# Performance work log

Measured on AMD Instinct MI355X. Metric: run time of the kernel, lower is better.

The kernel has to match this reference:

```python
import jax, jax.numpy as jnp
import numpy as np
from jax import lax

EPS = 1e-5  # BatchNorm eps (eval mode, running stats)
HEADS = 8

# --- surrogate-gradient Heaviside (sigmoid surrogate, alpha=4) ---
@jax.custom_vjp
def spike(u):
    return (u >= 0.0).astype(u.dtype)

def _spike_fwd(u):
    return spike(u), u

def _spike_bwd(u, g):
    s = jax.nn.sigmoid(4.0 * u)
    return (g * 4.0 * s * (1.0 - s),)

spike.defvjp(_spike_fwd, _spike_bwd)

def lif(x, tau=0.5, threshold=1.0):
    """Multi-step LIF over leading time axis: v_t = tau*v_{t-1} + x_t,
    s_t = H(v_t - threshold), hard reset v_t *= (1 - s_t)."""
    def step(v, xt):
        v = tau * v + xt
        s = spike(v - threshold)
        return v * (1.0 - s), s
    _, out = lax.scan(step, jnp.zeros_like(x[0]), x)
    return out

def bn_eval(x, gamma, beta, mean, var):
    # x: (T,B,C,N); per-channel affine using running stats
    inv = gamma / jnp.sqrt(var + EPS)
    return x * inv[None, None, :, None] + (beta - mean * inv)[None, None, :, None]

def setup_inputs() -> dict:
    key = jax.random.key(0)
    ks = jax.random.split(key, 12)
    T, B, C, H, W = 4, 32, 384, 16, 16
    d = {}
    d['x'] = jax.random.normal(ks[0], (T, B, C, H, W), dtype=jnp.float32)
    # 1x1 Conv1d weights == (C_out, C_in) matrices
    sc = 1.0 / np.sqrt(C)
    d['q_w'] = jax.random.normal(ks[1], (C, C), dtype=jnp.float32) * sc
    d['q_gamma'] = jnp.ones((C,), jnp.float32)
    d['q_beta'] = jnp.zeros((C,), jnp.float32)
    d['q_mean'] = jax.random.normal(ks[2], (C,), dtype=jnp.float32) * 0.1
    d['q_var'] = jax.random.uniform(ks[3], (C,), dtype=jnp.float32) + 0.5
    d['k_w'] = jax.random.normal(ks[4], (C, C), dtype=jnp.float32) * sc
    d['k_gamma'] = jnp.ones((C,), jnp.float32)
    d['k_beta'] = jnp.zeros((C,), jnp.float32)
    d['k_mean'] = jax.random.normal(ks[5], (C,), dtype=jnp.float32) * 0.1
    d['k_var'] = jax.random.uniform(ks[6], (C,), dtype=jnp.float32) + 0.5
    d['proj_w'] = jax.random.normal(ks[7], (C, C), dtype=jnp.float32) * sc
    d['proj_b'] = jax.random.normal(ks[8], (C,), dtype=jnp.float32) * 0.01
    d['proj_gamma'] = jnp.ones((C,), jnp.float32)
    d['proj_beta'] = jnp.zeros((C,), jnp.float32)
    d['proj_mean'] = jax.random.normal(ks[9], (C,), dtype=jnp.float32) * 0.1
    d['proj_var'] = jax.random.uniform(ks[10], (C,), dtype=jnp.float32) + 0.5
    d['mem_alpha'] = jnp.float32(0.2)
    return d

def reference(x, q_w, q_gamma, q_beta, q_mean, q_var,
              k_w, k_gamma, k_beta, k_mean, k_var,
              proj_w, proj_b, proj_gamma, proj_beta, proj_mean, proj_var,
              mem_alpha):
    T, B, C, H, W = x.shape
    Hh = HEADS
    Dh = C // Hh
    N = H * W
    # proj_lif applied to raw input, then flatten spatial dims
    s = lif(x, tau=0.5, threshold=1.0).reshape(T, B, C, N)
    # q path: 1x1 conv (channel GEMM) -> BN -> LIF
    q = lif(bn_eval(jnp.einsum('tbcn,dc->tbdn', s, q_w), q_gamma, q_beta, q_mean, q_var),
            tau=0.5, threshold=1.0).reshape(T, B, Hh, Dh, N)
    # k path
    k = lif(bn_eval(jnp.einsum('tbcn,dc->tbdn', s, k_w), k_gamma, k_beta, k_mean, k_var),
            tau=0.5, threshold=1.0).reshape(T, B, Hh, Dh, N)
    # temporal decayed memory: m_0 = q_0; m_t = alpha*m_{t-1} + (1-alpha)*q_{t-1}
    def mstep(m_prev, q_prev):
        m = mem_alpha * m_prev + (1.0 - mem_alpha) * q_prev
        return m, m
    _, mems_rest = lax.scan(mstep, q[0], q[:-1])
    mems = jnp.concatenate([q[:1], mems_rest], axis=0)  # (T,B,Hh,Dh,N)
    # cat along Dh then sum == sum(mems)+sum(q)
    q_sum = jnp.sum(mems, axis=3, keepdims=True) + jnp.sum(q, axis=3, keepdims=True)
    attn = lif(q_sum, tau=0.5, threshold=0.5)  # (T,B,Hh,1,N)
    y = (attn * k).reshape(T, B, C, N)
    # proj conv (with bias) -> BN -> reshape back to (T,B,C,H,W)
    y = jnp.einsum('tbcn,dc->tbdn', y, proj_w) + proj_b[None, None, :, None]
    y = bn_eval(y, proj_gamma, proj_beta, proj_mean, proj_var)
    return y.reshape(T, B, C, H, W)
```

## Files before the change

kernel.cpp:

```cpp
#include <hip/hip_runtime.h>

#define T_ 4
#define B_ 32
#define C_ 384
#define N_ 256
#define HEADS_ 8
#define DH_ 48
#define EPS_ 1e-5f
#define NW_ (C_*C_)

typedef _Float16 f16;
typedef __attribute__((ext_vector_type(8))) _Float16 f16x8;
typedef __attribute__((ext_vector_type(16))) float f32x16;

#define PSCALE     4096.0f
#define PSCALE_INV (1.0f/4096.0f)
#define SPIKE_BYTE 0x3Cu

__device__ __forceinline__ void unpack4(unsigned int w, unsigned int& lo, unsigned int& hi) {
#if defined(__has_builtin) && __has_builtin(__builtin_amdgcn_perm)
    lo = __builtin_amdgcn_perm(w, w, 0x010C000Cu);
    hi = __builtin_amdgcn_perm(w, w, 0x030C020Cu);
#else
    lo = ((w & 0xFFu) << 8) | ((w & 0xFF00u) << 16);
    hi = ((w & 0x00FF0000u) >> 8) | (w & 0xFF000000u);
#endif
}

__device__ __forceinline__ void unpack16(uint4 w, uint4& o0, uint4& o1) {
    unpack4(w.x, o0.x, o0.y); unpack4(w.y, o0.z, o0.w);
    unpack4(w.z, o1.x, o1.y); unpack4(w.w, o1.z, o1.w);
}

__device__ __forceinline__ void wsplit(float w, f16& a, f16& b) {
    a = (f16)w; b = (f16)((w - (float)a) * PSCALE);
}

__global__ __launch_bounds__(256)
void prep_kernel(const float* __restrict__ x, unsigned char* __restrict__ s,
                 const float* __restrict__ qw, const float* __restrict__ kw,
                 const float* __restrict__ pw,
                 f16* __restrict__ q2, f16* __restrict__ k2, f16* __restrict__ p2)
{
    if (blockIdx.z >= 32) {
        const int blid = ((blockIdx.z - 32) * 3 + blockIdx.y) * 4 + blockIdx.x;
        const int i4 = blid * 256 + threadIdx.x;
        {
            float4 w = ((const float4*)qw)[i4];
            union { f16 h[4]; uint2 u; } a, b;
            wsplit(w.x, a.h[0], b.h[0]); wsplit(w.y, a.h[1], b.h[1]);
            wsplit(w.z, a.h[2], b.h[2]); wsplit(w.w, a.h[3], b.h[3]);
            *(uint2*)&q2[(size_t)i4 * 4] = a.u;
            *(uint2*)&q2[NW_ + (size_t)i4 * 4] = b.u;
        }
        {
            float4 w = ((const float4*)kw)[i4];
            union { f16 h[4]; uint2 u; } a, b;
            wsplit(w.x, a.h[0], b.h[0]); wsplit(w.y, a.h[1], b.h[1]);
            wsplit(w.z, a.h[2], b.h[2]); wsplit(w.w, a.h[3], b.h[3]);
            *(uint2*)&k2[(size_t)i4 * 4] = a.u;
            *(uint2*)&k2[NW_ + (size_t)i4 * 4] = b.u;
        }
        {
            float4 w = ((const float4*)pw)[i4];
            union { f16 h[4]; uint2 u; } a, b;
            wsplit(w.x, a.h[0], b.h[0]); wsplit(w.y, a.h[1], b.h[1]);
            wsplit(w.z, a.h[2], b.h[2]); wsplit(w.w, a.h[3], b.h[3]);
            *(uint2*)&p2[(size_t)i4 * 4] = a.u;
            *(uint2*)&p2[NW_ + (size_t)i4 * 4] = b.u;
        }
        return;
    }

    const int tid = threadIdx.x;
    const int ng = tid & 15;
    const int cg = tid >> 4;
    const int n4 = blockIdx.x * 64 + ng * 4;
    const int c0 = blockIdx.y * 128 + cg * 8;
    const int b  = blockIdx.z;

    float v[8][4];
#pragma unroll
    for (int i = 0; i < 8; ++i)
#pragma unroll
        for (int j = 0; j < 4; ++j) v[i][j] = 0.f;

#pragma unroll
    for (int t = 0; t < T_; ++t) {
        const float* xt = x + (((size_t)t * B_ + b) * C_) * N_;
        float4 xv[8];
#pragma unroll
        for (int i = 0; i < 8; ++i)
            xv[i] = *(const float4*)&xt[(size_t)(c0 + i) * N_ + n4];
#pragma unroll
        for (int j = 0; j < 4; ++j) {
            union { unsigned char bb[8]; uint2 u; } u;
#pragma unroll
            for (int i = 0; i < 8; ++i) {
                float xa = (j == 0) ? xv[i].x : (j == 1) ? xv[i].y
                         : (j == 2) ? xv[i].z : xv[i].w;
                float vv = 0.5f * v[i][j] + xa;
                int sp = (vv >= 1.0f) ? 1 : 0;
                v[i][j] = sp ? 0.f : vv;
                u.bb[i] = sp ? (unsigned char)SPIKE_BYTE : (unsigned char)0;
            }
            unsigned char* dst = s + (((size_t)t * B_ + b) * N_ + n4 + j) * (size_t)C_ + c0;
            *(uint2*)dst = u.u;
        }
    }
}

__global__ __launch_bounds__(256)
void qk_gemm_lif_kernel(const f16* __restrict__ Wq, const f16* __restrict__ Wk,
                        const unsigned char* __restrict__ S,
                        const float* __restrict__ qg, const float* __restrict__ qb,
                        const float* __restrict__ qm, const float* __restrict__ qv,
                        const float* __restrict__ kg, const float* __restrict__ kb,
                        const float* __restrict__ km, const float* __restrict__ kv,
                        unsigned char* __restrict__ q_spk,
                        unsigned char* __restrict__ k_spk)
{
    __shared__ __align__(16) char smem[36864];
    f16 (*As)[72]      = reinterpret_cast<f16(*)[72]>(smem);
    f16 (*Bs)[64][72]  = reinterpret_cast<f16(*)[64][72]>(smem + 18432);

    const int tid  = threadIdx.x;
    const int lane = tid & 63;
    const int wave = tid >> 6;
    const int wm = wave & 1, wd = wave >> 1;
    const int l31 = lane & 31;
    const int lhi = lane >> 5;

    const int mb = blockIdx.x;
    const int b  = mb >> 3;
    const int n0 = (mb & 7) * 32;
    const int dp0 = blockIdx.y * 64;
    const int path = (dp0 >= C_) ? 1 : 0;
    const int d0 = dp0 - path * C_;

    const f16* W = path ? Wk : Wq;
    const float* g_  = path ? kg : qg;
    const float* be_ = path ? kb : qb;
    const float* m_  = path ? km : qm;
    const float* va_ = path ? kv : qv;
    unsigned char* spk = path ? k_spk : q_spk;

    const int dcol = d0 + wd * 32 + l31;
    const float inv = g_[dcol] / sqrtf(va_[dcol] + EPS_);
    const float add = be_[dcol] - m_[dcol] * inv;

    const int ar = tid >> 1;
    const int ah = (tid & 1) * 32;
    const int at = ar >> 5;
    const int anl = ar & 31;
    const unsigned char* arow = S + (((size_t)at * B_ + b) * N_ + n0 + anl) * (size_t)C_;
    const int aps = 4 * anl + ((at + (anl >> 1)) & 3);

    const int bp = tid >> 7;
    const int brr = (tid >> 1) & 63;
    const int bh = (tid & 1) * 32;
    const f16* brow = W + (size_t)bp * NW_ + (size_t)(d0 + brr) * C_;

    const int abase = 4 * (l31 >> 2) + ((l31 + (l31 >> 3)) & 3);
    const f16* pa0 = &As[wm * 64 + abase][0];
    const f16* pa1 = pa0 + 32 * 72;

    f32x16 acc[2][2];
#pragma unroll
    for (int ms = 0; ms < 2; ++ms)
#pragma unroll
        for (int p = 0; p < 2; ++p)
#pragma unroll
            for (int r = 0; r < 16; ++r) acc[ms][p][r] = 0.f;

    uint4 ra0 = *(const uint4*)(arow + ah);
    uint4 ra1 = *(const uint4*)(arow + ah + 16);
    uint4 rb0 = *(const uint4*)(brow + bh);
    uint4 rb1 = *(const uint4*)(brow + bh + 8);
    uint4 rb2 = *(const uint4*)(brow + bh + 16);
    uint4 rb3 = *(const uint4*)(brow + bh + 24);

#pragma unroll
    for (int ic = 0; ic < 6; ++ic) {
        __syncthreads();
        {
            uint4 o0, o1;
            unpack16(ra0, o0, o1);
            *(uint4*)&As[aps][ah]      = o0;
            *(uint4*)&As[aps][ah + 8]  = o1;
            unpack16(ra1, o0, o1);
            *(uint4*)&As[aps][ah + 16] = o0;
            *(uint4*)&As[aps][ah + 24] = o1;
            *(uint4*)&Bs[bp][brr][bh]      = rb0;
            *(uint4*)&Bs[bp][brr][bh + 8]  = rb1;
            *(uint4*)&Bs[bp][brr][bh + 16] = rb2;
            *(uint4*)&Bs[bp][brr][bh + 24] = rb3;
        }
        __syncthreads();
        if (ic < 5) {
            const int kn = ic * 64 + 64;
            ra0 = *(const uint4*)(arow + kn + ah);
            ra1 = *(const uint4*)(arow + kn + ah + 16);
            rb0 = *(const uint4*)(brow + kn + bh);
            rb1 = *(const uint4*)(brow + kn + bh + 8);
            rb2 = *(const uint4*)(brow + kn + bh + 16);
            rb3 = *(const uint4*)(brow + kn + bh + 24);
        }
#pragma unroll
        for (int kk = 0; kk < 4; ++kk) {
            const int ko = kk * 16 + lhi * 8;
            f16x8 a0 = *(const f16x8*)(pa0 + ko);
            f16x8 a1 = *(const f16x8*)(pa1 + ko);
            f16x8 b0 = *(const f16x8*)&Bs[0][wd * 32 + l31][ko];
            f16x8 b1 = *(const f16x8*)&Bs[1][wd * 32 + l31][ko];
            acc[0][0] = __builtin_amdgcn_mfma_f32_32x32x16_f16(a0, b0, acc[0][0], 0, 0, 0);
            acc[1][0] = __builtin_amdgcn_mfma_f32_32x32x16_f16(a1, b0, acc[1][0], 0, 0, 0);
            acc[0][1] = __builtin_amdgcn_mfma_f32_32x32x16_f16(a0, b1, acc[0][1], 0, 0, 0);
            acc[1][1] = __builtin_amdgcn_mfma_f32_32x32x16_f16(a1, b1, acc[1][1], 0, 0, 0);
        }
    }

#pragma unroll
    for (int ms = 0; ms < 2; ++ms)
#pragma unroll
    for (int g = 0; g < 4; ++g) {
        const int n = n0 + wm * 16 + ms * 8 + 2 * g + lhi;
        float v = 0.f;
#pragma unroll
        for (int t = 0; t < 4; ++t) {
            const int r = g * 4 + t;
            float val = (acc[ms][0][r] + acc[ms][1][r] * PSCALE_INV) * inv + add;
            float vv = 0.5f * v + val;
            int sp = (vv >= 1.0f) ? 1 : 0;
            v = sp ? 0.f : vv;
            spk[(((size_t)t * B_ + b) * N_ + n) * C_ + dcol] =
                sp ? (unsigned char)SPIKE_BYTE : (unsigned char)0;
        }
    }
}

__global__ __launch_bounds__(256)
void head_attn_kernel(const unsigned char* __restrict__ q_spk,
                      const float* __restrict__ alpha_p,
                      unsigned char* __restrict__ attn)
{
    int i = blockIdx.x * 256 + threadIdx.x;
    int n = i & (N_ - 1);
    int h = (i >> 8) & (HEADS_ - 1);
    int b = i >> 11;
    const float alpha = alpha_p[0];
    const int stride = B_ * HEADS_ * N_;
    float M = 0.f, v = 0.f, Sprev = 0.f;
#pragma unroll
    for (int t = 0; t < T_; ++t) {
        const uint4* p = (const uint4*)(q_spk + (((size_t)(t * B_ + b) * N_) + n) * C_ + h * DH_);
        int cnt = 0;
#pragma unroll
        for (int j = 0; j < 3; ++j) {
            uint4 w = p[j];
            cnt += __popc(w.x & 0x04040404u) + __popc(w.y & 0x04040404u)
                 + __popc(w.z & 0x04040404u) + __popc(w.w & 0x04040404u);
        }
        float Sqt = (float)cnt;
        if (t == 0) M = Sqt;
        else        M = alpha * M + (1.f - alpha) * Sprev;
        float qsum = M + Sqt;
        float vv = 0.5f * v + qsum;
        unsigned char sp = (vv >= 0.5f) ? 1 : 0;
        v = sp ? 0.f : vv;
        attn[(size_t)t * stride + i] = sp;
        Sprev = Sqt;
    }
}

__global__ __launch_bounds__(256)
void proj_gemm_kernel(const f16* __restrict__ Wp,
                      const unsigned char* __restrict__ K8,
                      const unsigned char* __restrict__ attn,
                      const float* __restrict__ bias,
                      const float* __restrict__ gamma, const float* __restrict__ beta,
                      const float* __restrict__ mean,  const float* __restrict__ var,
                      float* __restrict__ out)
{
    __shared__ __align__(16) char smem[36864];
    f16 (*As)[72]     = reinterpret_cast<f16(*)[72]>(smem);
    f16 (*Bs)[64][72] = reinterpret_cast<f16(*)[64][72]>(smem + 18432);

    const int tid  = threadIdx.x;
    const int lane = tid & 63;
    const int wave = tid >> 6;
    const int wm = wave & 1, wd = wave >> 1;
    const int l31 = lane & 31;
    const int lhi = lane >> 5;

    const int mb = blockIdx.x;
    const int tb = mb >> 1;
    const int n0 = (mb & 1) * 128;
    const int d0 = blockIdx.y * 64;

    const int dcol = d0 + wd * 32 + l31;
    const float iv = gamma[dcol] / sqrtf(var[dcol] + EPS_);
    const float ad = beta[dcol] - mean[dcol] * iv + bias[dcol] * iv;

    const int ar = tid >> 1;
    const int ah = (tid & 1) * 32;
    const int an = n0 + ar;
    const unsigned char* arow = K8 + ((size_t)tb * N_ + an) * (size_t)C_;
    const unsigned char* At = attn + (size_t)tb * HEADS_ * N_;

    const int bp = tid >> 7;
    const int brr = (tid >> 1) & 63;
    const int bh = (tid & 1) * 32;
    const f16* brow = Wp + (size_t)bp * NW_ + (size_t)(d0 + brr) * C_;

    f32x16 acc[2][2];
#pragma unroll
    for (int ms = 0; ms < 2; ++ms)
#pragma unroll
        for (int p = 0; p < 2; ++p)
#pragma unroll
            for (int r = 0; r < 16; ++r) acc[ms][p][r] = 0.f;

    uint2 wa0, wa1, wa2, wa3;
    unsigned char am0, am1, am2, am3;
    uint4 rb0, rb1, rb2, rb3;
    {
        const int c0 = ah;
        am0 = At[(size_t)((c0     ) / DH_) * N_ + an]; wa0 = *(const uint2*)(arow + c0);
        am1 = At[(size_t)((c0 +  8) / DH_) * N_ + an]; wa1 = *(const uint2*)(arow + c0 + 8);
        am2 = At[(size_t)((c0 + 16) / DH_) * N_ + an]; wa2 = *(const uint2*)(arow + c0 + 16);
        am3 = At[(size_t)((c0 + 24) / DH_) * N_ + an]; wa3 = *(const uint2*)(arow + c0 + 24);
        rb0 = *(const uint4*)(brow + bh);
        rb1 = *(const uint4*)(brow + bh + 8);
        rb2 = *(const uint4*)(brow + bh + 16);
        rb3 = *(const uint4*)(brow + bh + 24);
    }

#pragma unroll
    for (int ic = 0; ic < 6; ++ic) {
        __syncthreads();
        {
            uint2 w;
            uint4 o;
            w = am0 ? wa0 : make_uint2(0u, 0u);
            unpack4(w.x, o.x, o.y); unpack4(w.y, o.z, o.w);
            *(uint4*)&As[ar][ah] = o;
            w = am1 ? wa1 : make_uint2(0u, 0u);
            unpack4(w.x, o.x, o.y); unpack4(w.y, o.z, o.w);
            *(uint4*)&As[ar][ah + 8] = o;
            w = am2 ? wa2 : make_uint2(0u, 0u);
            unpack4(w.x, o.x, o.y); unpack4(w.y, o.z, o.w);
            *(uint4*)&As[ar][ah + 16] = o;
            w = am3 ? wa3 : make_uint2(0u, 0u);
            unpack4(w.x, o.x, o.y); unpack4(w.y, o.z, o.w);
            *(uint4*)&As[ar][ah + 24] = o;
            *(uint4*)&Bs[bp][brr][bh]      = rb0;
            *(uint4*)&Bs[bp][brr][bh + 8]  = rb1;
            *(uint4*)&Bs[bp][brr][bh + 16] = rb2;
            *(uint4*)&Bs[bp][brr][bh + 24] = rb3;
        }
        __syncthreads();
        if (ic < 5) {
            const int kn = ic * 64 + 64;
            const int c0 = kn + ah;
            am0 = At[(size_t)((c0     ) / DH_) * N_ + an]; wa0 = *(const uint2*)(arow + c0);
            am1 = At[(size_t)((c0 +  8) / DH_) * N_ + an]; wa1 = *(const uint2*)(arow + c0 + 8);
            am2 = At[(size_t)((c0 + 16) / DH_) * N_ + an]; wa2 = *(const uint2*)(arow + c0 + 16);
            am3 = At[(size_t)((c0 + 24) / DH_) * N_ + an]; wa3 = *(const uint2*)(arow + c0 + 24);
            rb0 = *(const uint4*)(brow + kn + bh);
            rb1 = *(const uint4*)(brow + kn + bh + 8);
            rb2 = *(const uint4*)(brow + kn + bh + 16);
            rb3 = *(const uint4*)(brow + kn + bh + 24);
        }
#pragma unroll
        for (int kk = 0; kk < 4; ++kk) {
            const int ko = kk * 16 + lhi * 8;
            f16x8 a0 = *(const f16x8*)&As[wm * 64 + l31][ko];
            f16x8 a1 = *(const f16x8*)&As[wm * 64 + 32 + l31][ko];
            f16x8 b0 = *(const f16x8*)&Bs[0][wd * 32 + l31][ko];
            f16x8 b1 = *(const f16x8*)&Bs[1][wd * 32 + l31][ko];
            acc[0][0] = __builtin_amdgcn_mfma_f32_32x32x16_f16(a0, b0, acc[0][0], 0, 0, 0);
            acc[1][0] = __builtin_amdgcn_mfma_f32_32x32x16_f16(a1, b0, acc[1][0], 0, 0, 0);
            acc[0][1] = __builtin_amdgcn_mfma_f32_32x32x16_f16(a0, b1, acc[0][1], 0, 0, 0);
            acc[1][1] = __builtin_amdgcn_mfma_f32_32x32x16_f16(a1, b1, acc[1][1], 0, 0, 0);
        }
    }

    float* obase = out + ((size_t)tb * C_ + dcol) * N_;
#pragma unroll
    for (int ms = 0; ms < 2; ++ms)
#pragma unroll
    for (int r = 0; r < 16; ++r) {
        int n = n0 + wm * 64 + ms * 32 + (r & 3) + 8 * (r >> 2) + 4 * lhi;
        float val = acc[ms][0][r] + acc[ms][1][r] * PSCALE_INV;
        obase[n] = val * iv + ad;
    }
}

extern "C" void kernel_launch(void* const* d_in, const int* in_sizes, int n_in,
                              void* d_out, int out_size, void* d_ws, size_t ws_size,
                              hipStream_t stream)
{
    const float* x       = (const float*)d_in[0];
    const float* q_w     = (const float*)d_in[1];
    const float* q_gamma = (const float*)d_in[2];
    const float* q_beta  = (const float*)d_in[3];
    const float* q_mean  = (const float*)d_in[4];
    const float* q_var   = (const float*)d_in[5];
    const float* k_w     = (const float*)d_in[6];
    const float* k_gamma = (const float*)d_in[7];
    const float* k_beta  = (const float*)d_in[8];
    const float* k_mean  = (const float*)d_in[9];
    const float* k_var   = (const float*)d_in[10];
    const float* proj_w  = (const float*)d_in[11];
    const float* proj_b  = (const float*)d_in[12];
    const float* p_gamma = (const float*)d_in[13];
    const float* p_beta  = (const float*)d_in[14];
    const float* p_mean  = (const float*)d_in[15];
    const float* p_var   = (const float*)d_in[16];
    const float* m_alpha = (const float*)d_in[17];

    float* out = (float*)d_out;

    const size_t SPK_BYTES = (size_t)T_ * B_ * N_ * C_;
    const size_t W2_BYTES  = (size_t)2 * NW_ * sizeof(f16);
    const size_t TBHN      = (size_t)T_ * B_ * HEADS_ * N_;

    unsigned char* ws = (unsigned char*)d_ws;
    size_t off = 0;
    auto carve = [&](size_t bytes) {
        off = (off + 255) & ~(size_t)255;
        void* p = ws + off;
        off += bytes;
        return p;
    };
    unsigned char* s_u8  = (unsigned char*)carve(SPK_BYTES);
    unsigned char* q_spk = (unsigned char*)carve(SPK_BYTES);
    unsigned char* k_spk = (unsigned char*)carve(SPK_BYTES);
    f16* Wq2    = (f16*)carve(W2_BYTES);
    f16* Wk2    = (f16*)carve(W2_BYTES);
    f16* Wp2    = (f16*)carve(W2_BYTES);
    unsigned char* attn = (unsigned char*)carve(TBHN);

    dim3 pgrid1(4, 3, 44);
    prep_kernel<<<pgrid1, 256, 0, stream>>>(x, s_u8, q_w, k_w, proj_w,
                                            Wq2, Wk2, Wp2);

    dim3 qkgrid(256, 12);
    qk_gemm_lif_kernel<<<qkgrid, 256, 0, stream>>>(Wq2, Wk2, s_u8,
                                                   q_gamma, q_beta, q_mean, q_var,
                                                   k_gamma, k_beta, k_mean, k_var,
                                                   q_spk, k_spk);

    head_attn_kernel<<<(B_ * HEADS_ * N_) / 256, 256, 0, stream>>>(q_spk, m_alpha, attn);

    dim3 pjgrid(256, 6);
    proj_gemm_kernel<<<pjgrid, 256, 0, stream>>>(Wp2, k_spk, attn, proj_b,
                                                 p_gamma, p_beta, p_mean, p_var, out);
}
```

Before: 206.8 us.

## Store q spikes head-contiguous and stage projection output through LDS

The q-path spike tensor is now written in a (T,B,HEADS,N,DH) layout. Each head_attn thread can then read its 48 spike bytes as one contiguous run instead of indexing into the channel-major layout. The projection GEMM epilogue now writes its results to an LDS tile first, then emits coalesced float4 global stores along N, replacing strided scalar stores. The LDS tile uses a 129-float row pitch to avoid bank conflicts, which leaves the float4 LDS reads not 16-byte aligned; this may cost performance or need unaligned-access support.

```diff
diff --git a/kernel.cpp b/kernel.cpp
--- a/kernel.cpp
+++ b/kernel.cpp
@@ -143,7 +143,6 @@
     const float* be_ = path ? kb : qb;
     const float* m_  = path ? km : qm;
     const float* va_ = path ? kv : qv;
-    unsigned char* spk = path ? k_spk : q_spk;
 
     const int dcol = d0 + wd * 32 + l31;
     const float inv = g_[dcol] / sqrtf(va_[dcol] + EPS_);
@@ -220,21 +219,43 @@
         }
     }
 
-#pragma unroll
-    for (int ms = 0; ms < 2; ++ms)
-#pragma unroll
-    for (int g = 0; g < 4; ++g) {
-        const int n = n0 + wm * 16 + ms * 8 + 2 * g + lhi;
-        float v = 0.f;
-#pragma unroll
-        for (int t = 0; t < 4; ++t) {
-            const int r = g * 4 + t;
-            float val = (acc[ms][0][r] + acc[ms][1][r] * PSCALE_INV) * inv + add;
-            float vv = 0.5f * v + val;
-            int sp = (vv >= 1.0f) ? 1 : 0;
-            v = sp ? 0.f : vv;
-            spk[(((size_t)t * B_ + b) * N_ + n) * C_ + dcol] =
-                sp ? (unsigned char)SPIKE_BYTE : (unsigned char)0;
+    if (path == 0) {
+        const int hq = dcol / DH_;
+        const int dh = dcol - hq * DH_;
+#pragma unroll
+        for (int ms = 0; ms < 2; ++ms)
+#pragma unroll
+        for (int g = 0; g < 4; ++g) {
+            const int n = n0 + wm * 16 + ms * 8 + 2 * g + lhi;
+            float v = 0.f;
+#pragma unroll
+            for (int t = 0; t < 4; ++t) {
+                const int r = g * 4 + t;
+                float val = (acc[ms][0][r] + acc[ms][1][r] * PSCALE_INV) * inv + add;
+                float vv = 0.5f * v + val;
+                int sp = (vv >= 1.0f) ? 1 : 0;
+                v = sp ? 0.f : vv;
+                q_spk[((((size_t)t * B_ + b) * HEADS_ + hq) * N_ + n) * DH_ + dh] =
+                    sp ? (unsigned char)SPIKE_BYTE : (unsigned char)0;
+            }
+        }
+    } else {
+#pragma unroll
+        for (int ms = 0; ms < 2; ++ms)
+#pragma unroll
+        for (int g = 0; g < 4; ++g) {
+            const int n = n0 + wm * 16 + ms * 8 + 2 * g + lhi;
+            float v = 0.f;
+#pragma unroll
+            for (int t = 0; t < 4; ++t) {
+                const int r = g * 4 + t;
+                float val = (acc[ms][0][r] + acc[ms][1][r] * PSCALE_INV) * inv + add;
+                float vv = 0.5f * v + val;
+                int sp = (vv >= 1.0f) ? 1 : 0;
+                v = sp ? 0.f : vv;
+                k_spk[(((size_t)t * B_ + b) * N_ + n) * C_ + dcol] =
+                    sp ? (unsigned char)SPIKE_BYTE : (unsigned char)0;
+            }
         }
     }
 }
@@ -245,15 +266,12 @@
                       unsigned char* __restrict__ attn)
 {
     int i = blockIdx.x * 256 + threadIdx.x;
-    int n = i & (N_ - 1);
-    int h = (i >> 8) & (HEADS_ - 1);
-    int b = i >> 11;
     const float alpha = alpha_p[0];
     const int stride = B_ * HEADS_ * N_;
     float M = 0.f, v = 0.f, Sprev = 0.f;
 #pragma unroll
     for (int t = 0; t < T_; ++t) {
-        const uint4* p = (const uint4*)(q_spk + (((size_t)(t * B_ + b) * N_) + n) * C_ + h * DH_);
+        const uint4* p = (const uint4*)(q_spk + ((size_t)t * stride + i) * DH_);
         int cnt = 0;
 #pragma unroll
         for (int j = 0; j < 3; ++j) {
@@ -285,6 +303,7 @@
     __shared__ __align__(16) char smem[36864];
     f16 (*As)[72]     = reinterpret_cast<f16(*)[72]>(smem);
     f16 (*Bs)[64][72] = reinterpret_cast<f16(*)[64][72]>(smem + 18432);
+    float (*Pt)[129]  = reinterpret_cast<float(*)[129]>(smem);
 
     const int tid  = threadIdx.x;
     const int lane = tid & 63;
@@ -386,14 +405,27 @@
         }
     }
 
-    float* obase = out + ((size_t)tb * C_ + dcol) * N_;
-#pragma unroll
-    for (int ms = 0; ms < 2; ++ms)
-#pragma unroll
-    for (int r = 0; r < 16; ++r) {
-        int n = n0 + wm * 64 + ms * 32 + (r & 3) + 8 * (r >> 2) + 4 * lhi;
-        float val = acc[ms][0][r] + acc[ms][1][r] * PSCALE_INV;
-        obase[n] = val * iv + ad;
+    __syncthreads();
+    {
+        const int dl = wd * 32 + l31;
+#pragma unroll
+        for (int ms = 0; ms < 2; ++ms)
+#pragma unroll
+        for (int r = 0; r < 16; ++r) {
+            const int nl = wm * 64 + ms * 32 + (r & 3) + 8 * (r >> 2) + 4 * lhi;
+            Pt[dl][nl] = (acc[ms][0][r] + acc[ms][1][r] * PSCALE_INV) * iv + ad;
+        }
+    }
+    __syncthreads();
+    {
+        const int col4 = (tid & 31) * 4;
+        const int rw   = tid >> 5;
+#pragma unroll
+        for (int it = 0; it < 8; ++it) {
+            const int row = rw + it * 8;
+            float4 vv = *(const float4*)&Pt[row][col4];
+            *(float4*)&out[((size_t)tb * C_ + d0 + row) * N_ + n0 + col4] = vv;
+        }
     }
 }
 
```

Result: faster. 200.7 us (-2.9%).
